# Performance work log

Hardware: AMD Instinct MI355X
Metric: run time of the kernel (lower is better)

## Reference

```python
import jax, jax.numpy as jnp
import numpy as np

EMBED_DIM = 256
NUM_HEADS = 8


def positional_encoding(max_seq_len, embed_dim):
    # Faithful to torch source: exponent uses 2*i/embed_dim with raw column index i;
    # row 0 is all zeros; sin on even cols, cos on odd cols for rows 1:.
    pos = jnp.arange(max_seq_len, dtype=jnp.float32)[:, None]          # [L,1]
    i = jnp.arange(embed_dim, dtype=jnp.float32)[None, :]              # [1,D]
    angles = pos / jnp.power(10000.0, 2.0 * i / embed_dim)             # [L,D]
    pe = jnp.where((jnp.arange(embed_dim) % 2 == 0)[None, :],
                   jnp.sin(angles), jnp.cos(angles))
    pe = pe.at[0].set(0.0)
    return pe


def setup_inputs() -> dict:
    key = jax.random.key(0)
    ks = jax.random.split(key, 9)
    b, c, h, w = 4, EMBED_DIM, 48, 48
    d = EMBED_DIM  # internal_dim (downsample_rate=1)
    s = 1.0 / np.sqrt(d)
    inp = {
        "x": jax.random.normal(ks[0], (b, c, h, w), dtype=jnp.float32),
        "wq": jax.random.uniform(ks[1], (d, d), jnp.float32, -s, s),
        "bq": jax.random.uniform(ks[2], (d,), jnp.float32, -s, s),
        "wk": jax.random.uniform(ks[3], (d, d), jnp.float32, -s, s),
        "bk": jax.random.uniform(ks[4], (d,), jnp.float32, -s, s),
        "wv": jax.random.uniform(ks[5], (d, d), jnp.float32, -s, s),
        "bv": jax.random.uniform(ks[6], (d,), jnp.float32, -s, s),
        "wo": jax.random.uniform(ks[7], (d, d), jnp.float32, -s, s),
        "bo": jax.random.uniform(ks[8], (d,), jnp.float32, -s, s),
    }
    return inp


def reference(x, wq, bq, wk, bk, wv, bv, wo, bo):
    b, c, h, w = x.shape
    n = h * w
    H = NUM_HEADS
    dh = c // H
    xs = x.reshape(b, c, n).transpose(0, 2, 1)            # [b, n, c]
    xs = xs + positional_encoding(n, c)[None]             # add PE
    q = xs @ wq.T + bq                                    # [b, n, c]
    k = xs @ wk.T + bk
    v = xs @ wv.T + bv
    # separate heads -> [b, H, n, dh]
    q = q.reshape(b, n, H, dh).transpose(0, 2, 1, 3)
    k = k.reshape(b, n, H, dh).transpose(0, 2, 1, 3)
    v = v.reshape(b, n, H, dh).transpose(0, 2, 1, 3)
    attn = jnp.einsum("bhqd,bhkd->bhqk", q, k) / jnp.sqrt(jnp.float32(dh))
    attn = jax.nn.softmax(attn, axis=-1)
    out = jnp.einsum("bhqk,bhkd->bhqd", attn, v)          # [b, H, n, dh]
    out = out.transpose(0, 2, 1, 3).reshape(b, n, c)      # recombine heads
    out = out @ wo.T + bo                                 # out_proj
    return out.transpose(0, 2, 1).reshape(b, c, h, w)
```

## Files before the change

### kernel.cpp

```cpp
#include <hip/hip_runtime.h>

#define EMBED 256
#define NPOS  2304
#define BATCH 4
#define NH    8
#define DH    32

typedef float f32x4  __attribute__((ext_vector_type(4)));
typedef short bf16x8 __attribute__((ext_vector_type(8)));
typedef short s16x4  __attribute__((ext_vector_type(4)));
typedef unsigned u32x4 __attribute__((ext_vector_type(4)));

static __device__ __forceinline__ short f2b(float f) {
    union { float f; unsigned u; } c; c.f = f;
    unsigned r = (c.u + 0x7FFFu + ((c.u >> 16) & 1u)) >> 16;
    return (short)r;
}

static __device__ __forceinline__ unsigned cvtpk(float lo, float hi) {
    unsigned r;
    asm("v_cvt_pk_bf16_f32 %0, %1, %2" : "=v"(r) : "v"(lo), "v"(hi));
    return r;
}

static __device__ __forceinline__ float fexp2(float x) {
    float r;
    asm("v_exp_f32 %0, %1" : "=v"(r) : "v"(x));
    return r;
}

static __device__ __forceinline__ void plswap32(unsigned& a, unsigned& b) {
    asm("v_permlane32_swap_b32 %0, %1" : "+v"(a), "+v"(b));
}
static __device__ __forceinline__ void plswap16(unsigned& a, unsigned& b) {
    asm("v_permlane16_swap_b32 %0, %1" : "+v"(a), "+v"(b));
}

static __device__ __forceinline__ void gl_lds16(const short* g, short* l) {
    __builtin_amdgcn_global_load_lds(
        (const __attribute__((address_space(1))) unsigned int*)(g),
        (__attribute__((address_space(3))) unsigned int*)(l),
        16, 0, 0);
}

__global__ __launch_bounds__(256) void prep_all(
        const float* __restrict__ x,
        const float* __restrict__ wq, const float* __restrict__ wk,
        const float* __restrict__ wv, const float* __restrict__ wo,
        short* __restrict__ wqkv, short* __restrict__ wob,
        short* __restrict__ xs) {
    __shared__ float xt[32][65];
    int blk = blockIdx.x;
    int t = threadIdx.x;
    if (blk < 1024) {
        int g = blk * 256 + t;
        if (g < 196608) {
            int j = g >> 8, kk = g & 255;
            int proj = j >> 8, jj = j & 255;
            const float* s = (proj == 0) ? wq : (proj == 1) ? wk : wv;
            wqkv[g] = f2b(s[jj * 256 + kk]);
        } else if (g < 262144) {
            int h2 = g - 196608;
            wob[h2] = f2b(wo[h2]);
        }
        return;
    }
    int bx = blk - 1024;
    int b = bx / 288, rem = bx % 288;
    int c0 = (rem / 36) * 32, pos0 = (rem % 36) * 64;
    int j = t & 63, i0 = t >> 6;
    const float* xp = x + (size_t)(b * EMBED + c0) * NPOS + pos0;
#pragma unroll
    for (int rr = 0; rr < 8; ++rr) {
        int i = rr * 4 + i0;
        xt[i][j] = xp[(size_t)i * NPOS + j];
    }
    __syncthreads();
    int ii = (t & 15) * 2, jj0 = t >> 4;
    const float kln = -0.07195578415606394f;
#pragma unroll
    for (int pp = 0; pp < 4; ++pp) {
        int jj = pp * 16 + jj0;
        int pos = pos0 + jj;
        float v0 = xt[ii][jj], v1 = xt[ii + 1][jj];
        float pe0 = 0.f, pe1 = 0.f;
        if (pos > 0) {
            int c = c0 + ii;
            float a0 = (float)pos * __expf((float)c * kln);
            float a1 = (float)pos * __expf((float)(c + 1) * kln);
            pe0 = __sinf(a0);
            pe1 = __cosf(a1);
        }
        unsigned lo = (unsigned short)f2b(v0 + pe0);
        unsigned hi = (unsigned short)f2b(v1 + pe1);
        *reinterpret_cast<unsigned*>(xs + (size_t)(b * NPOS + pos) * EMBED + c0 + ii) =
            lo | (hi << 16);
    }
}

__global__ __launch_bounds__(256) void gemm_qkv(
        const short* __restrict__ A, const short* __restrict__ Bw,
        const float* __restrict__ bq, const float* __restrict__ bk,
        const float* __restrict__ bv,
        short* __restrict__ qd, short* __restrict__ kd, short* __restrict__ vtd) {
    __shared__ short a_sm[64 * 32];
    __shared__ short b_sm[64 * 32];
    int bx = blockIdx.x;
    int bm = bx / 12, bn = bx % 12;
    int m0 = bm * 64, n0 = bn * 64;
    int t = threadIdx.x;
    int lane = t & 63, wid = t >> 6;
    int wm = wid >> 1, wn = wid & 1;
    int l15 = lane & 15, l4 = lane >> 4;

    f32x4 acc[2][2];
#pragma unroll
    for (int ni = 0; ni < 2; ++ni) {
        int jcol = n0 + wn * 32 + ni * 16 + l15;
        int proj = jcol >> 8, jj = jcol & 255;
        float bias = ((proj == 0) ? bq : (proj == 1) ? bk : bv)[jj];
        f32x4 bi = {bias, bias, bias, bias};
        acc[0][ni] = bi;
        acc[1][ni] = bi;
    }

    int srow = t >> 2, sblk = t & 3;
    int ssw = (sblk ^ ((srow >> 1) & 3)) * 8;
    const short* ag = &A[(size_t)(m0 + srow) * 256 + sblk * 8];
    const short* bg = &Bw[(size_t)(n0 + srow) * 256 + sblk * 8];
    short* al = &a_sm[srow * 32 + ssw];
    short* bl = &b_sm[srow * 32 + ssw];

    for (int ks = 0; ks < 8; ++ks) {
        __syncthreads();
        *(bf16x8*)al = *(const bf16x8*)(ag + ks * 32);
        *(bf16x8*)bl = *(const bf16x8*)(bg + ks * 32);
        __syncthreads();
        bf16x8 af[2], bf[2];
#pragma unroll
        for (int mi = 0; mi < 2; ++mi) {
            int ar = wm * 32 + mi * 16 + l15;
            af[mi] = *(const bf16x8*)&a_sm[ar * 32 + ((l4 ^ ((ar >> 1) & 3)) * 8)];
        }
#pragma unroll
        for (int ni = 0; ni < 2; ++ni) {
            int br = wn * 32 + ni * 16 + l15;
            bf[ni] = *(const bf16x8*)&b_sm[br * 32 + ((l4 ^ ((br >> 1) & 3)) * 8)];
        }
#pragma unroll
        for (int mi = 0; mi < 2; ++mi)
#pragma unroll
            for (int ni = 0; ni < 2; ++ni)
                acc[mi][ni] = __builtin_amdgcn_mfma_f32_16x16x32_bf16(
                    af[mi], bf[ni], acc[mi][ni], 0, 0, 0);
    }

    const float qs = 0.2550348623f;
#pragma unroll
    for (int mi = 0; mi < 2; ++mi) {
        int rowb = m0 + wm * 32 + mi * 16 + l4 * 4;
        int b = rowb / NPOS;
        int pos = rowb - b * NPOS;
#pragma unroll
        for (int ni = 0; ni < 2; ++ni) {
            int jcol = n0 + wn * 32 + ni * 16 + l15;
            int proj = jcol >> 8, jj = jcol & 255;
            int h = jj >> 5, d = jj & 31;
            if (proj == 2) {
                s16x4 pk;
#pragma unroll
                for (int r = 0; r < 4; ++r) pk[r] = f2b(acc[mi][ni][r]);
                *(s16x4*)&vtd[((size_t)(b * NH + h) * DH + d) * NPOS + pos] = pk;
            } else {
                short* dst = (proj == 0) ? qd : kd;
                float sc = (proj == 0) ? qs : 1.0f;
#pragma unroll
                for (int r = 0; r < 4; ++r)
                    dst[((size_t)(b * NH + h) * NPOS + pos + r) * DH + d] =
                        f2b(acc[mi][ni][r] * sc);
            }
        }
    }
}


__global__ __launch_bounds__(256) void attn_fwd(
        const short* __restrict__ Q, const short* __restrict__ K,
        const short* __restrict__ VT, short* __restrict__ AO) {
    __shared__ short smem[20480];

    int bx0 = blockIdx.x;
    int bx = (bx0 & 7) * 144 + (bx0 >> 3);
    int bh = bx / 36, qg = bx % 36;
    int q0 = qg * 64;
    int t = threadIdx.x, lane = t & 63, wid = t >> 6;
    int l15 = lane & 15, l4 = lane >> 4;

    const short* Qb = Q + ((size_t)bh * NPOS + q0) * DH;
    bf16x8 qf[4];
#pragma unroll
    for (int qt = 0; qt < 4; ++qt)
        qf[qt] = *(const bf16x8*)&Qb[(qt * 16 + l15) * DH + l4 * 8];

    int kv0 = wid * 576;
    int ra = lane >> 2, blk = lane & 3;
    int swzk = (ra >> 1) & 3;
    int swzv = (ra & 3) ^ ((ra >> 2) & 3);
    const short* kga = K + ((size_t)bh * NPOS + kv0 + ra) * DH + ((blk ^ swzk) * 8);
    const short* vga = VT + ((size_t)bh * DH + ra) * NPOS + kv0 + ((blk ^ swzv) * 8);

    short* kbuf = smem + wid * 5120;
    short* vbuf = kbuf + 2048;

#pragma unroll
    for (int p = 0; p < 2; ++p) {
        gl_lds16(kga + p * 1024,            kbuf + p * 1024);
        gl_lds16(kga + p * 1024 + 16 * DH,  kbuf + p * 1024 + 512);
        gl_lds16(vga + p * 32,              vbuf + p * 1024);
        gl_lds16(vga + p * 32 + 16 * NPOS,  vbuf + p * 1024 + 512);
    }

    f32x4 zero = {0.f, 0.f, 0.f, 0.f};
    f32x4 o[2][4];
#pragma unroll
    for (int qt = 0; qt < 4; ++qt) { o[0][qt] = zero; o[1][qt] = zero; }
    float ls[4] = {0.f, 0.f, 0.f, 0.f};
    const float MB = -17.312340490667561f;
    const f32x4 mb = {MB, MB, MB, MB};

    int kswr = (l4 ^ ((l15 >> 1) & 3)) * 8;
    int vswr = (l4 ^ ((l15 & 3) ^ ((l15 >> 2) & 3))) * 8;

#pragma unroll 1
    for (int tt = 0; tt < 18; ++tt) {
        int buf = tt & 1;
        if (tt < 17) asm volatile("s_waitcnt vmcnt(4)" ::: "memory");
        else         asm volatile("s_waitcnt vmcnt(0)" ::: "memory");

        const short* kb = kbuf + buf * 1024;
        const short* vb = vbuf + buf * 1024;
        bf16x8 kf0 = *(const bf16x8*)&kb[l15 * 32 + kswr];
        bf16x8 kf1 = *(const bf16x8*)&kb[(16 + l15) * 32 + kswr];
        bf16x8 vf0 = *(const bf16x8*)&vb[l15 * 32 + vswr];
        bf16x8 vf1 = *(const bf16x8*)&vb[(16 + l15) * 32 + vswr];
        asm volatile("s_waitcnt lgkmcnt(0)" ::: "memory");
        __builtin_amdgcn_sched_barrier(0);

        if (tt + 2 < 18) {
            gl_lds16(kga + (tt + 2) * 1024,            kbuf + buf * 1024);
            gl_lds16(kga + (tt + 2) * 1024 + 16 * DH,  kbuf + buf * 1024 + 512);
            gl_lds16(vga + (tt + 2) * 32,              vbuf + buf * 1024);
            gl_lds16(vga + (tt + 2) * 32 + 16 * NPOS,  vbuf + buf * 1024 + 512);
        }

#pragma unroll
        for (int qt = 0; qt < 4; ++qt) {
            f32x4 s0 = __builtin_amdgcn_mfma_f32_16x16x32_bf16(kf0, qf[qt], mb, 0, 0, 0);
            f32x4 s1 = __builtin_amdgcn_mfma_f32_16x16x32_bf16(kf1, qf[qt], mb, 0, 0, 0);

            float e00 = fexp2(s0[0]), e01 = fexp2(s0[1]), e02 = fexp2(s0[2]), e03 = fexp2(s0[3]);
            float e10 = fexp2(s1[0]), e11 = fexp2(s1[1]), e12 = fexp2(s1[2]), e13 = fexp2(s1[3]);
            ls[qt] += ((e00 + e01) + (e02 + e03)) + ((e10 + e11) + (e12 + e13));

            unsigned p00 = cvtpk(e00, e01), p01 = cvtpk(e02, e03);
            unsigned p10 = cvtpk(e10, e11), p11 = cvtpk(e12, e13);
            unsigned a0 = p00, b0 = p10;
            plswap32(a0, b0); plswap16(a0, b0);
            unsigned a1 = p01, b1 = p11;
            plswap32(a1, b1); plswap16(a1, b1);
            u32x4 fr = {a0, a1, b0, b1};
            bf16x8 pf = __builtin_bit_cast(bf16x8, fr);

            o[0][qt] = __builtin_amdgcn_mfma_f32_16x16x32_bf16(vf0, pf, o[0][qt], 0, 0, 0);
            o[1][qt] = __builtin_amdgcn_mfma_f32_16x16x32_bf16(vf1, pf, o[1][qt], 0, 0, 0);
        }
    }

#pragma unroll
    for (int qt = 0; qt < 4; ++qt) {
        ls[qt] += __shfl_xor(ls[qt], 16);
        ls[qt] += __shfl_xor(ls[qt], 32);
    }

    if (wid > 0) {
        f32x4* od = (f32x4*)(smem + wid * 5120);
        float* ld = (float*)(smem + wid * 5120 + 4096);
#pragma unroll
        for (int qt = 0; qt < 4; ++qt) {
            ld[qt * 64 + lane] = ls[qt];
#pragma unroll
            for (int dt = 0; dt < 2; ++dt)
                od[(qt * 2 + dt) * 64 + lane] = o[dt][qt];
        }
    }
    __syncthreads();
    if (wid == 0) {
        int b = bh >> 3, h = bh & 7;
#pragma unroll
        for (int qt = 0; qt < 4; ++qt) {
            float lt = ls[qt];
#pragma unroll
            for (int w = 1; w < 4; ++w)
                lt += ((float*)(smem + w * 5120 + 4096))[qt * 64 + lane];
            float inv = __builtin_amdgcn_rcpf(lt);
            int qrow = q0 + qt * 16 + l15;
            size_t obase = ((size_t)b * NPOS + qrow) * EMBED + h * DH;
#pragma unroll
            for (int dt = 0; dt < 2; ++dt) {
                f32x4 ot = o[dt][qt];
#pragma unroll
                for (int w = 1; w < 4; ++w)
                    ot += ((f32x4*)(smem + w * 5120))[(qt * 2 + dt) * 64 + lane];
                unsigned x0 = cvtpk(ot[0] * inv, ot[1] * inv);
                unsigned x1 = cvtpk(ot[2] * inv, ot[3] * inv);
                *(unsigned long long*)&AO[obase + dt * 16 + l4 * 4] =
                    (unsigned long long)x0 | ((unsigned long long)x1 << 32);
            }
        }
    }
}

__global__ __launch_bounds__(256) void gemm_out(
        const short* __restrict__ A, const short* __restrict__ Bw,
        const float* __restrict__ bo, float* __restrict__ out) {
    __shared__ short a_sm[32 * 32];
    __shared__ short b_sm[64 * 32];
    int bx = blockIdx.x;
    int bm = bx >> 2, bn = bx & 3;
    int m0 = bm * 32, n0 = bn * 64;
    int t = threadIdx.x;
    int lane = t & 63, wid = t >> 6;
    int wm = wid >> 1, wn = wid & 1;
    int l15 = lane & 15, l4 = lane >> 4;

    f32x4 acc[2];
#pragma unroll
    for (int ni = 0; ni < 2; ++ni) {
        float bias = bo[n0 + wn * 32 + ni * 16 + l15];
        f32x4 bi = {bias, bias, bias, bias};
        acc[ni] = bi;
    }

    int srow = t >> 2, sblk = t & 3;
    int ssw = (sblk ^ ((srow >> 1) & 3)) * 8;
    const short* ag = &A[(size_t)(m0 + srow) * 256 + sblk * 8];
    const short* bg = &Bw[(size_t)(n0 + srow) * 256 + sblk * 8];
    short* al = &a_sm[srow * 32 + ssw];
    short* bl = &b_sm[srow * 32 + ssw];

    for (int ks = 0; ks < 8; ++ks) {
        __syncthreads();
        if (t < 128) *(bf16x8*)al = *(const bf16x8*)(ag + ks * 32);
        *(bf16x8*)bl = *(const bf16x8*)(bg + ks * 32);
        __syncthreads();
        int ar = wm * 16 + l15;
        bf16x8 af = *(const bf16x8*)&a_sm[ar * 32 + ((l4 ^ ((ar >> 1) & 3)) * 8)];
        bf16x8 bf[2];
#pragma unroll
        for (int ni = 0; ni < 2; ++ni) {
            int br = wn * 32 + ni * 16 + l15;
            bf[ni] = *(const bf16x8*)&b_sm[br * 32 + ((l4 ^ ((br >> 1) & 3)) * 8)];
        }
#pragma unroll
        for (int ni = 0; ni < 2; ++ni)
            acc[ni] = __builtin_amdgcn_mfma_f32_16x16x32_bf16(af, bf[ni], acc[ni], 0, 0, 0);
    }

    int rowb = m0 + wm * 16 + l4 * 4;
    int b = rowb / NPOS;
    int pos = rowb - b * NPOS;
#pragma unroll
    for (int ni = 0; ni < 2; ++ni) {
        int jcol = n0 + wn * 32 + ni * 16 + l15;
        *(f32x4*)&out[((size_t)(b * EMBED) + jcol) * NPOS + pos] = acc[ni];
    }
}

extern "C" void kernel_launch(void* const* d_in, const int* in_sizes, int n_in,
                              void* d_out, int out_size, void* d_ws, size_t ws_size,
                              hipStream_t stream) {
    const float* x  = (const float*)d_in[0];
    const float* wq = (const float*)d_in[1];
    const float* bq = (const float*)d_in[2];
    const float* wk = (const float*)d_in[3];
    const float* bk = (const float*)d_in[4];
    const float* wv = (const float*)d_in[5];
    const float* bv = (const float*)d_in[6];
    const float* wo = (const float*)d_in[7];
    const float* bo = (const float*)d_in[8];

    char* ws = (char*)d_ws;
    short* wqkv = (short*)(ws);
    short* wob  = (short*)(ws + 393216);
    short* xs   = (short*)(ws + 524288);
    short* qb   = (short*)(ws + 5242880);
    short* kb   = (short*)(ws + 9961472);
    short* vtb  = (short*)(ws + 14680064);
    short* ao   = (short*)(ws + 19398656);
    float* out  = (float*)d_out;

    hipLaunchKernelGGL(prep_all, dim3(2176), dim3(256), 0, stream,
                       x, wq, wk, wv, wo, wqkv, wob, xs);
    hipLaunchKernelGGL(gemm_qkv, dim3(1728), dim3(256), 0, stream,
                       xs, wqkv, bq, bk, bv, qb, kb, vtb);
    hipLaunchKernelGGL(attn_fwd, dim3(1152), dim3(256), 0, stream, qb, kb, vtb, ao);
    hipLaunchKernelGGL(gemm_out, dim3(1152), dim3(256), 0, stream, ao, wob, bo, out);
}
```

Baseline: 71.62 us.

## Convert weights to bf16 inside GEMM loaders and compute softmax row sums via MFMA

Drops the separate weight-conversion pass from the prep kernel. The QKV and output GEMMs now load fp32 weights and pack them to bf16 in registers before the LDS store. Separately, the attention kernel replaces the per-thread exp summation and cross-lane shuffles with an extra MFMA against a ones vector to accumulate row sums. This trims prep work and VALU adds, but doubles weight read bytes in every GEMM block and adds one MFMA per tile.

```diff
diff --git a/kernel.cpp b/kernel.cpp
--- a/kernel.cpp
+++ b/kernel.cpp
@@ -43,29 +43,11 @@
         16, 0, 0);
 }
 
-__global__ __launch_bounds__(256) void prep_all(
-        const float* __restrict__ x,
-        const float* __restrict__ wq, const float* __restrict__ wk,
-        const float* __restrict__ wv, const float* __restrict__ wo,
-        short* __restrict__ wqkv, short* __restrict__ wob,
-        short* __restrict__ xs) {
+__global__ __launch_bounds__(256) void build_xs(
+        const float* __restrict__ x, short* __restrict__ xs) {
     __shared__ float xt[32][65];
-    int blk = blockIdx.x;
+    int bx = blockIdx.x;
     int t = threadIdx.x;
-    if (blk < 1024) {
-        int g = blk * 256 + t;
-        if (g < 196608) {
-            int j = g >> 8, kk = g & 255;
-            int proj = j >> 8, jj = j & 255;
-            const float* s = (proj == 0) ? wq : (proj == 1) ? wk : wv;
-            wqkv[g] = f2b(s[jj * 256 + kk]);
-        } else if (g < 262144) {
-            int h2 = g - 196608;
-            wob[h2] = f2b(wo[h2]);
-        }
-        return;
-    }
-    int bx = blk - 1024;
     int b = bx / 288, rem = bx % 288;
     int c0 = (rem / 36) * 32, pos0 = (rem % 36) * 64;
     int j = t & 63, i0 = t >> 6;
@@ -99,7 +81,9 @@
 }
 
 __global__ __launch_bounds__(256) void gemm_qkv(
-        const short* __restrict__ A, const short* __restrict__ Bw,
+        const short* __restrict__ A,
+        const float* __restrict__ wq, const float* __restrict__ wk,
+        const float* __restrict__ wv,
         const float* __restrict__ bq, const float* __restrict__ bk,
         const float* __restrict__ bv,
         short* __restrict__ qd, short* __restrict__ kd, short* __restrict__ vtd) {
@@ -127,14 +111,20 @@
     int srow = t >> 2, sblk = t & 3;
     int ssw = (sblk ^ ((srow >> 1) & 3)) * 8;
     const short* ag = &A[(size_t)(m0 + srow) * 256 + sblk * 8];
-    const short* bg = &Bw[(size_t)(n0 + srow) * 256 + sblk * 8];
+    int jcolB = n0 + srow;
+    int projB = jcolB >> 8, jjB = jcolB & 255;
+    const float* wsrc = ((projB == 0) ? wq : (projB == 1) ? wk : wv) + jjB * 256 + sblk * 8;
     short* al = &a_sm[srow * 32 + ssw];
     short* bl = &b_sm[srow * 32 + ssw];
 
     for (int ks = 0; ks < 8; ++ks) {
         __syncthreads();
         *(bf16x8*)al = *(const bf16x8*)(ag + ks * 32);
-        *(bf16x8*)bl = *(const bf16x8*)(bg + ks * 32);
+        f32x4 w0 = *(const f32x4*)(wsrc + ks * 32);
+        f32x4 w1 = *(const f32x4*)(wsrc + ks * 32 + 4);
+        u32x4 wp = {cvtpk(w0[0], w0[1]), cvtpk(w0[2], w0[3]),
+                    cvtpk(w1[0], w1[1]), cvtpk(w1[2], w1[3])};
+        *(bf16x8*)bl = __builtin_bit_cast(bf16x8, wp);
         __syncthreads();
         bf16x8 af[2], bf[2];
 #pragma unroll
@@ -222,11 +212,13 @@
 
     f32x4 zero = {0.f, 0.f, 0.f, 0.f};
     f32x4 o[2][4];
-#pragma unroll
-    for (int qt = 0; qt < 4; ++qt) { o[0][qt] = zero; o[1][qt] = zero; }
-    float ls[4] = {0.f, 0.f, 0.f, 0.f};
+    f32x4 lacc[4];
+#pragma unroll
+    for (int qt = 0; qt < 4; ++qt) { o[0][qt] = zero; o[1][qt] = zero; lacc[qt] = zero; }
     const float MB = -17.312340490667561f;
     const f32x4 mb = {MB, MB, MB, MB};
+    const u32x4 ones_u = {0x3F803F80u, 0x3F803F80u, 0x3F803F80u, 0x3F803F80u};
+    const bf16x8 ones = __builtin_bit_cast(bf16x8, ones_u);
 
     int kswr = (l4 ^ ((l15 >> 1) & 3)) * 8;
     int vswr = (l4 ^ ((l15 & 3) ^ ((l15 >> 2) & 3))) * 8;
@@ -260,7 +252,6 @@
 
             float e00 = fexp2(s0[0]), e01 = fexp2(s0[1]), e02 = fexp2(s0[2]), e03 = fexp2(s0[3]);
             float e10 = fexp2(s1[0]), e11 = fexp2(s1[1]), e12 = fexp2(s1[2]), e13 = fexp2(s1[3]);
-            ls[qt] += ((e00 + e01) + (e02 + e03)) + ((e10 + e11) + (e12 + e13));
 
             unsigned p00 = cvtpk(e00, e01), p01 = cvtpk(e02, e03);
             unsigned p10 = cvtpk(e10, e11), p11 = cvtpk(e12, e13);
@@ -273,21 +264,17 @@
 
             o[0][qt] = __builtin_amdgcn_mfma_f32_16x16x32_bf16(vf0, pf, o[0][qt], 0, 0, 0);
             o[1][qt] = __builtin_amdgcn_mfma_f32_16x16x32_bf16(vf1, pf, o[1][qt], 0, 0, 0);
-        }
-    }
-
-#pragma unroll
-    for (int qt = 0; qt < 4; ++qt) {
-        ls[qt] += __shfl_xor(ls[qt], 16);
-        ls[qt] += __shfl_xor(ls[qt], 32);
-    }
+            lacc[qt] = __builtin_amdgcn_mfma_f32_16x16x32_bf16(ones, pf, lacc[qt], 0, 0, 0);
+        }
+    }
+
 
     if (wid > 0) {
         f32x4* od = (f32x4*)(smem + wid * 5120);
         float* ld = (float*)(smem + wid * 5120 + 4096);
 #pragma unroll
         for (int qt = 0; qt < 4; ++qt) {
-            ld[qt * 64 + lane] = ls[qt];
+            ld[qt * 64 + lane] = lacc[qt][0];
 #pragma unroll
             for (int dt = 0; dt < 2; ++dt)
                 od[(qt * 2 + dt) * 64 + lane] = o[dt][qt];
@@ -298,7 +285,7 @@
         int b = bh >> 3, h = bh & 7;
 #pragma unroll
         for (int qt = 0; qt < 4; ++qt) {
-            float lt = ls[qt];
+            float lt = lacc[qt][0];
 #pragma unroll
             for (int w = 1; w < 4; ++w)
                 lt += ((float*)(smem + w * 5120 + 4096))[qt * 64 + lane];
@@ -321,7 +308,7 @@
 }
 
 __global__ __launch_bounds__(256) void gemm_out(
-        const short* __restrict__ A, const short* __restrict__ Bw,
+        const short* __restrict__ A, const float* __restrict__ wo,
         const float* __restrict__ bo, float* __restrict__ out) {
     __shared__ short a_sm[32 * 32];
     __shared__ short b_sm[64 * 32];
@@ -344,14 +331,18 @@
     int srow = t >> 2, sblk = t & 3;
     int ssw = (sblk ^ ((srow >> 1) & 3)) * 8;
     const short* ag = &A[(size_t)(m0 + srow) * 256 + sblk * 8];
-    const short* bg = &Bw[(size_t)(n0 + srow) * 256 + sblk * 8];
+    const float* wsrc = wo + (size_t)(n0 + srow) * 256 + sblk * 8;
     short* al = &a_sm[srow * 32 + ssw];
     short* bl = &b_sm[srow * 32 + ssw];
 
     for (int ks = 0; ks < 8; ++ks) {
         __syncthreads();
         if (t < 128) *(bf16x8*)al = *(const bf16x8*)(ag + ks * 32);
-        *(bf16x8*)bl = *(const bf16x8*)(bg + ks * 32);
+        f32x4 w0 = *(const f32x4*)(wsrc + ks * 32);
+        f32x4 w1 = *(const f32x4*)(wsrc + ks * 32 + 4);
+        u32x4 wp = {cvtpk(w0[0], w0[1]), cvtpk(w0[2], w0[3]),
+                    cvtpk(w1[0], w1[1]), cvtpk(w1[2], w1[3])};
+        *(bf16x8*)bl = __builtin_bit_cast(bf16x8, wp);
         __syncthreads();
         int ar = wm * 16 + l15;
         bf16x8 af = *(const bf16x8*)&a_sm[ar * 32 + ((l4 ^ ((ar >> 1) & 3)) * 8)];
@@ -390,19 +381,16 @@
     const float* bo = (const float*)d_in[8];
 
     char* ws = (char*)d_ws;
-    short* wqkv = (short*)(ws);
-    short* wob  = (short*)(ws + 393216);
-    short* xs   = (short*)(ws + 524288);
-    short* qb   = (short*)(ws + 5242880);
-    short* kb   = (short*)(ws + 9961472);
-    short* vtb  = (short*)(ws + 14680064);
-    short* ao   = (short*)(ws + 19398656);
-    float* out  = (float*)d_out;
-
-    hipLaunchKernelGGL(prep_all, dim3(2176), dim3(256), 0, stream,
-                       x, wq, wk, wv, wo, wqkv, wob, xs);
+    short* xs  = (short*)(ws);
+    short* qb  = (short*)(ws + 4718592);
+    short* kb  = (short*)(ws + 9437184);
+    short* vtb = (short*)(ws + 14155776);
+    short* ao  = (short*)(ws + 18874368);
+    float* out = (float*)d_out;
+
+    hipLaunchKernelGGL(build_xs, dim3(1152), dim3(256), 0, stream, x, xs);
     hipLaunchKernelGGL(gemm_qkv, dim3(1728), dim3(256), 0, stream,
-                       xs, wqkv, bq, bk, bv, qb, kb, vtb);
+                       xs, wq, wk, wv, bq, bk, bv, qb, kb, vtb);
     hipLaunchKernelGGL(attn_fwd, dim3(1152), dim3(256), 0, stream, qb, kb, vtb, ao);
-    hipLaunchKernelGGL(gemm_out, dim3(1152), dim3(256), 0, stream, ao, wob, bo, out);
-}
+    hipLaunchKernelGGL(gemm_out, dim3(1152), dim3(256), 0, stream, ao, wo, bo, out);
+}
```

Result: no change. 72.91 us (+1.8%).
